# Performance work log

Measured on AMD Instinct MI355X. Metric: run time of the kernel, lower is better.

Reference implementation:

```python
import jax, jax.numpy as jnp
import numpy as np

GRID = 300  # NaiveFourierKANLayer default gridsize
EPS = 1e-5


def layer_norm(x, w, b):
    mu = jnp.mean(x, axis=-1, keepdims=True)
    var = jnp.var(x, axis=-1, keepdims=True)
    return (x - mu) * jax.lax.rsqrt(var + EPS) * w + b


def fourier_kan(x, coeffs, bias):
    # x: [..., I], coeffs: [2, O, I, G], bias: [1, O]
    shp = x.shape
    I = shp[-1]
    xf = x.reshape(-1, I)
    k = jnp.arange(1, GRID + 1, dtype=x.dtype)           # [G]
    arg = xf[:, :, None] * k                             # [B, I, G]
    y = jnp.einsum('big,oig->bo', jnp.cos(arg), coeffs[0])
    y = y + jnp.einsum('big,oig->bo', jnp.sin(arg), coeffs[1])
    y = y + bias                                         # bias broadcasts [1, O]
    return y.reshape(shp[:-1] + (coeffs.shape[1],))


def setup_inputs() -> dict:
    key = jax.random.key(0)
    ks = jax.random.split(key, 4)
    B, N, D = 8, 196, 128          # batch, in_channels, in_dim
    O1 = 2 * D                     # amplifier out_dim
    x = jax.random.normal(ks[0], (B, N, D), dtype=jnp.float32)
    fc1_coeffs = jax.random.normal(ks[1], (2, O1, D, GRID), dtype=jnp.float32) / np.sqrt(D * GRID)
    fc2_coeffs = jax.random.normal(ks[2], (2, N, N, GRID), dtype=jnp.float32) / np.sqrt(N * GRID)
    return {
        'x': x,
        'ln1_w': jnp.ones((D,), jnp.float32),
        'ln1_b': jnp.zeros((D,), jnp.float32),
        'fc1_coeffs': fc1_coeffs,
        'fc1_bias': jnp.zeros((1, O1), jnp.float32),
        'ln2_w': jnp.ones((O1,), jnp.float32),
        'ln2_b': jnp.zeros((O1,), jnp.float32),
        'fc2_coeffs': fc2_coeffs,
        'fc2_bias': jnp.zeros((1, N), jnp.float32),
    }


def reference(x, ln1_w, ln1_b, fc1_coeffs, fc1_bias, ln2_w, ln2_b, fc2_coeffs, fc2_bias):
    B, N, D = x.shape
    # amplifier: LN over in_dim, FourierKAN in_dim -> 2*in_dim
    h = fourier_kan(layer_norm(x, ln1_w, ln1_b), fc1_coeffs, fc1_bias)   # [B, N, 2D]
    # channel_mix: LN over 2*in_dim, transpose, FourierKAN over channels, transpose back
    h = layer_norm(h, ln2_w, ln2_b)
    h = jnp.transpose(h, (0, 2, 1))                                      # [B, 2D, N]
    h = fourier_kan(h, fc2_coeffs, fc2_bias)                             # [B, 2D, N]
    h = jnp.transpose(h, (0, 2, 1))                                      # [B, N, 2D]
    return h.reshape(-1, 2 * N, D)                                       # [B, 2N, D]
```

## Files before the change

### kernel.cpp

```cpp
#include <hip/hip_runtime.h>
#include <math.h>

typedef short short8 __attribute__((ext_vector_type(8)));
typedef float f32x4 __attribute__((ext_vector_type(4)));

#define EPSF 1e-5f

union FragU { uint4 q; unsigned u[4]; short8 v; };

__device__ __forceinline__ unsigned pack_trunc2(float lo_val, float hi_val) {
    return __builtin_amdgcn_perm(__float_as_uint(hi_val), __float_as_uint(lo_val), 0x07060302u);
}
__device__ __forceinline__ float trunc_bf(float x) {
    return __uint_as_float(__float_as_uint(x) & 0xFFFF0000u);
}

__device__ __forceinline__ void gload16_lds(const void* g, void* l) {
    __builtin_amdgcn_global_load_lds(
        (const __attribute__((address_space(1))) void*)g,
        (__attribute__((address_space(3))) void*)l, 16, 0, 0);
}

#define PHASE_BAR() do { \
    asm volatile("s_waitcnt vmcnt(0)" ::: "memory"); \
    __builtin_amdgcn_s_barrier(); \
    __builtin_amdgcn_sched_barrier(0); \
    asm volatile("" ::: "memory"); \
} while (0)

__global__ void ln1_kernel(const float* __restrict__ x, const float* __restrict__ w,
                           const float* __restrict__ b, float* __restrict__ xnT) {
    int r = blockIdx.x;
    int t = threadIdx.x;
    const float* row = x + (size_t)r * 128;
    float v0 = row[t], v1 = row[t + 64];
    float s = v0 + v1, q = v0 * v0 + v1 * v1;
    #pragma unroll
    for (int off = 32; off > 0; off >>= 1) {
        s += __shfl_down(s, off);
        q += __shfl_down(q, off);
    }
    s = __shfl(s, 0); q = __shfl(q, 0);
    float mu = s * (1.f / 128.f);
    float var = q * (1.f / 128.f) - mu * mu;
    float rs = rsqrtf(var + EPSF);
    xnT[(size_t)t * 1792 + r]        = (v0 - mu) * rs * w[t]      + b[t];
    xnT[(size_t)(t + 64) * 1792 + r] = (v1 - mu) * rs * w[t + 64] + b[t + 64];
}

__launch_bounds__(256)
__global__ void fc1_kernel(const float* __restrict__ xnT, const float* __restrict__ coeffs,
                           float* __restrict__ h1, int KS) {
    const int nt = blockIdx.x;
    const int mt = blockIdx.y;
    const int ks = blockIdx.z;
    const int i0 = (ks * 128) / KS, i1 = ((ks + 1) * 128) / KS;
    const int t = threadIdx.x;
    const int wv = t >> 6, ln = t & 63;
    const int q = ln >> 4, col = ln & 15;
    const int mwrow = mt * 256 + wv * 64;

    __shared__ unsigned bhi[128 * 36];
    __shared__ unsigned blo[128 * 36];

    const float* c0 = coeffs;
    const float* c1 = coeffs + (size_t)256 * 128 * 300;

    f32x4 acc[4][8] = {};

    const int srow = t >> 1;
    const int j0 = (t & 1) * 16;
    const int og = nt * 128 + srow;
    const size_t prow = (size_t)og * 128;

    for (int i = i0; i < i1; ++i) {
        float zu[4];
        #pragma unroll
        for (int mf = 0; mf < 4; ++mf) {
            int m = mwrow + mf * 16 + col;
            zu[mf] = (m < 1568) ? xnT[(size_t)i * 1792 + m] : 0.f;
        }
        const float* p0 = c0 + (prow + i) * 300;
        const float* p1 = c1 + (prow + i) * 300;

        for (int c = 0; c < 10; ++c) {
            __syncthreads();
            {
                unsigned hw[16], lw[16];
                #pragma unroll
                for (int k4 = 0; k4 < 4; ++k4) {
                    int g = c * 32 + j0 + k4 * 4;
                    float w0[4], w1[4];
                    if (g + 4 <= 300) {
                        float4 a = *(const float4*)(p0 + g);
                        float4 bb = *(const float4*)(p1 + g);
                        w0[0]=a.x; w0[1]=a.y; w0[2]=a.z; w0[3]=a.w;
                        w1[0]=bb.x; w1[1]=bb.y; w1[2]=bb.z; w1[3]=bb.w;
                    } else {
                        #pragma unroll
                        for (int e = 0; e < 4; ++e) {
                            int gg = g + e; bool ok = gg < 300;
                            w0[e] = ok ? p0[gg] : 0.f;
                            w1[e] = ok ? p1[gg] : 0.f;
                        }
                    }
                    #pragma unroll
                    for (int e = 0; e < 4; ++e) {
                        hw[k4*4+e] = pack_trunc2(w0[e], w1[e]);
                        lw[k4*4+e] = pack_trunc2(w0[e]-trunc_bf(w0[e]), w1[e]-trunc_bf(w1[e]));
                    }
                }
                int base = srow * 36 + j0;
                *(uint4*)&bhi[base]      = make_uint4(hw[0], hw[1], hw[2], hw[3]);
                *(uint4*)&bhi[base + 4]  = make_uint4(hw[4], hw[5], hw[6], hw[7]);
                *(uint4*)&bhi[base + 8]  = make_uint4(hw[8], hw[9], hw[10], hw[11]);
                *(uint4*)&bhi[base + 12] = make_uint4(hw[12], hw[13], hw[14], hw[15]);
                *(uint4*)&blo[base]      = make_uint4(lw[0], lw[1], lw[2], lw[3]);
                *(uint4*)&blo[base + 4]  = make_uint4(lw[4], lw[5], lw[6], lw[7]);
                *(uint4*)&blo[base + 8]  = make_uint4(lw[8], lw[9], lw[10], lw[11]);
                *(uint4*)&blo[base + 12] = make_uint4(lw[12], lw[13], lw[14], lw[15]);
            }
            __syncthreads();
            #pragma unroll
            for (int h = 0; h < 2; ++h) {
                FragU ah[4], al[4];
                #pragma unroll
                for (int mf = 0; mf < 4; ++mf) {
                    #pragma unroll
                    for (int d = 0; d < 4; ++d) {
                        float kf = (float)(c * 32 + h * 16 + q * 4 + d + 1);
                        float a = zu[mf] * kf;
                        float cv = __cosf(a), sv = __sinf(a);
                        ah[mf].u[d] = pack_trunc2(cv, sv);
                        al[mf].u[d] = pack_trunc2(cv - trunc_bf(cv), sv - trunc_bf(sv));
                    }
                }
                #pragma unroll
                for (int nf = 0; nf < 8; ++nf) {
                    int addr = (nf * 16 + col) * 36 + h * 16 + q * 4;
                    FragU bh, bl;
                    bh.q = *(const uint4*)&bhi[addr];
                    bl.q = *(const uint4*)&blo[addr];
                    #pragma unroll
                    for (int mf = 0; mf < 4; ++mf) {
                        acc[mf][nf] = __builtin_amdgcn_mfma_f32_16x16x32_bf16(ah[mf].v, bh.v, acc[mf][nf], 0, 0, 0);
                        acc[mf][nf] = __builtin_amdgcn_mfma_f32_16x16x32_bf16(ah[mf].v, bl.v, acc[mf][nf], 0, 0, 0);
                        acc[mf][nf] = __builtin_amdgcn_mfma_f32_16x16x32_bf16(al[mf].v, bh.v, acc[mf][nf], 0, 0, 0);
                    }
                }
            }
        }
    }
    #pragma unroll
    for (int mf = 0; mf < 4; ++mf) {
        if (mwrow + mf * 16 >= 1568) continue;
        int mbase = mwrow + mf * 16 + q * 4;
        #pragma unroll
        for (int nf = 0; nf < 8; ++nf) {
            int o = nt * 128 + nf * 16 + col;
            #pragma unroll
            for (int r = 0; r < 4; ++r)
                atomicAdd(&h1[(size_t)(mbase + r) * 256 + o], acc[mf][nf][r]);
        }
    }
}

__global__ void ln2_kernel(const float* __restrict__ h1, const float* __restrict__ bias,
                           const float* __restrict__ w, const float* __restrict__ b,
                           float* __restrict__ h1n) {
    int r = blockIdx.x;
    int t = threadIdx.x;
    float v = h1[(size_t)r * 256 + t] + bias[t];
    float s = v, q = v * v;
    #pragma unroll
    for (int off = 32; off > 0; off >>= 1) {
        s += __shfl_down(s, off);
        q += __shfl_down(q, off);
    }
    __shared__ float ss[4], qq[4];
    int wid = t >> 6;
    if ((t & 63) == 0) { ss[wid] = s; qq[wid] = q; }
    __syncthreads();
    float S = ss[0] + ss[1] + ss[2] + ss[3];
    float Q = qq[0] + qq[1] + qq[2] + qq[3];
    float mu = S * (1.f / 256.f);
    float var = Q * (1.f / 256.f) - mu * mu;
    float rs = rsqrtf(var + EPSF);
    h1n[(size_t)r * 256 + t] = (v - mu) * rs * w[t] + b[t];
}

__device__ __forceinline__ void cmul(float& xr, float& xi, float br, float bi) {
    float nr = xr * br - xi * bi;
    float ni = xr * bi + xi * br;
    xr = nr; xi = ni;
}

__launch_bounds__(256, 2)
__global__ void fc2_kernel(const float* __restrict__ h1n, const float* __restrict__ coeffs,
                           float* __restrict__ out, int KS) {
    const int nt = blockIdx.x;
    const int b  = blockIdx.y;
    const int ks = blockIdx.z;
    const int i0 = (ks * 196) / KS, i1 = ((ks + 1) * 196) / KS;
    const int t = threadIdx.x;
    const int wv = t >> 6, ln = t & 63;
    const int q = ln >> 4, col = ln & 15;
    const int cwb = wv * 64;

    __shared__ float ldsf[2 * 2 * 4096];
    char* lds_raw = (char*)&ldsf[0];

    const float* d0 = coeffs;
    const float* d1 = coeffs + (size_t)196 * 196 * 300;

    f32x4 acc[4][8] = {};

    const int rb8  = ln >> 3;
    const int gsub = ((ln & 7) ^ rb8) * 4;
    const unsigned km = (q == 3) ? 0u : 0xFFFFFFFFu;

    auto STAGE = [&](int i, int c, int buf) {
        const int g = c * 32 + gsub;
        const size_t gw = (g + 4 <= 300) ? (size_t)g : 0;
        #pragma unroll
        for (int j = 0; j < 4; ++j) {
            int row = wv * 32 + j * 8 + rb8;
            int og = nt * 128 + row;
            if (og > 195) og = 195;
            size_t go = ((size_t)og * 196 + i) * 300 + gw;
            unsigned lo = (unsigned)buf * 32768u + (unsigned)wv * 4096u + (unsigned)j * 1024u;
            gload16_lds(d0 + go, lds_raw + lo);
            gload16_lds(d1 + go, lds_raw + lo + 16384);
        }
    };

    int cur = 0;
    STAGE(i0, 0, 0);
    for (int i = i0; i < i1; ++i) {
        float Rc[4], Rs[4], E1c[4], E1s[4], E13c[4], E13s[4];
        #pragma unroll
        for (int mf = 0; mf < 4; ++mf) {
            float x = h1n[((size_t)b * 196 + i) * 256 + cwb + mf * 16 + col];
            float c1_ = __cosf(x), s1_ = __sinf(x);
            float c2 = c1_*c1_ - s1_*s1_, s2 = 2.f*c1_*s1_;
            float c4 = c2*c2 - s2*s2,    s4 = 2.f*c2*s2;
            float c8 = c4*c4 - s4*s4,    s8 = 2.f*c4*s4;
            float c12 = c8*c4 - s8*s4,   s12 = c8*s4 + s8*c4;
            float c13 = c12*c1_ - s12*s1_, s13 = c12*s1_ + s12*c1_;
            float rc = c1_, rs = s1_;
            float m4c = (q & 1) ? c4 : 1.f, m4s = (q & 1) ? s4 : 0.f;
            cmul(rc, rs, m4c, m4s);
            float m8c = (q & 2) ? c8 : 1.f, m8s = (q & 2) ? s8 : 0.f;
            cmul(rc, rs, m8c, m8s);
            Rc[mf] = rc; Rs[mf] = rs;
            E1c[mf] = c1_; E1s[mf] = s1_;
            E13c[mf] = c13; E13s[mf] = s13;
        }
        for (int c = 0; c < 10; ++c) {
            PHASE_BAR();
            int ni = i, nc = c + 1;
            if (nc == 10) { nc = 0; ni = i + 1; }
            if (ni < i1) STAGE(ni, nc, cur ^ 1);
            __builtin_amdgcn_sched_barrier(0);
            __builtin_amdgcn_s_setprio(1);
            #pragma unroll
            for (int h = 0; h < 2; ++h) {
                if (h == 1 && c == 9) continue;
                FragU af[4];
                #pragma unroll
                for (int mf = 0; mf < 4; ++mf) {
                    #pragma unroll
                    for (int d = 0; d < 4; ++d) {
                        af[mf].u[d] = pack_trunc2(Rc[mf], Rs[mf]);
                        if (d < 3) cmul(Rc[mf], Rs[mf], E1c[mf], E1s[mf]);
                        else       cmul(Rc[mf], Rs[mf], E13c[mf], E13s[mf]);
                    }
                }
                #pragma unroll
                for (int nf = 0; nf < 8; ++nf) {
                    int row = nf * 16 + col;
                    int pb = cur * 32768 + row * 128 + (((h << 6) | (q << 4)) ^ ((col & 7) << 4));
                    float4 f0 = *(const float4*)(lds_raw + pb);
                    float4 f1 = *(const float4*)(lds_raw + pb + 16384);
                    FragU bf;
                    bf.u[0] = pack_trunc2(f0.x, f1.x);
                    bf.u[1] = pack_trunc2(f0.y, f1.y);
                    bf.u[2] = pack_trunc2(f0.z, f1.z);
                    bf.u[3] = pack_trunc2(f0.w, f1.w);
                    if (c == 9) {
                        bf.u[0] &= km; bf.u[1] &= km; bf.u[2] &= km; bf.u[3] &= km;
                    }
                    #pragma unroll
                    for (int mf = 0; mf < 4; ++mf)
                        acc[mf][nf] = __builtin_amdgcn_mfma_f32_16x16x32_bf16(af[mf].v, bf.v, acc[mf][nf], 0, 0, 0);
                }
            }
            __builtin_amdgcn_s_setprio(0);
            cur ^= 1;
        }
    }
    #pragma unroll
    for (int mf = 0; mf < 4; ++mf) {
        int cbase = cwb + mf * 16 + q * 4;
        #pragma unroll
        for (int nf = 0; nf < 8; ++nf) {
            int o = nt * 128 + nf * 16 + col;
            if (o < 196) {
                #pragma unroll
                for (int r = 0; r < 4; ++r)
                    atomicAdd(&out[((size_t)b * 196 + o) * 256 + cbase + r], acc[mf][nf][r]);
            }
        }
    }
}

__global__ void bias2_kernel(float* __restrict__ out, const float* __restrict__ bias) {
    int idx = blockIdx.x * 256 + threadIdx.x;
    int o = (idx >> 8) % 196;
    out[idx] += bias[o];
}

extern "C" void kernel_launch(void* const* d_in, const int* in_sizes, int n_in,
                              void* d_out, int out_size, void* d_ws, size_t ws_size,
                              hipStream_t stream) {
    const float* x       = (const float*)d_in[0];
    const float* ln1w    = (const float*)d_in[1];
    const float* ln1b    = (const float*)d_in[2];
    const float* fc1c    = (const float*)d_in[3];
    const float* fc1bias = (const float*)d_in[4];
    const float* ln2w    = (const float*)d_in[5];
    const float* ln2b    = (const float*)d_in[6];
    const float* fc2c    = (const float*)d_in[7];
    const float* fc2bias = (const float*)d_in[8];
    float* out = (float*)d_out;

    float* xnT = (float*)d_ws;
    float* h1  = xnT + 229376;
    float* h1n = h1 + 401408;

    hipMemsetAsync(h1, 0, (size_t)401408 * 4, stream);
    hipMemsetAsync(d_out, 0, (size_t)401408 * 4, stream);

    const int ks1 = 36, ks2 = 32;
    ln1_kernel<<<1568, 64, 0, stream>>>(x, ln1w, ln1b, xnT);
    fc1_kernel<<<dim3(2, 7, ks1), 256, 0, stream>>>(xnT, fc1c, h1, ks1);
    ln2_kernel<<<1568, 256, 0, stream>>>(h1, fc1bias, ln2w, ln2b, h1n);
    fc2_kernel<<<dim3(2, 8, ks2), 256, 0, stream>>>(h1n, fc2c, out, ks2);
    bias2_kernel<<<1568, 256, 0, stream>>>(out, fc2bias);
}
```

Measured before the change: 689.3 us.

## Double-buffer fc1 coefficient tiles via async global-to-LDS loads

Replaces the register-staged load, bf16-split and LDS store of the fc1 coefficients with direct global_load_lds transfers into a double-buffered, XOR-swizzled fp32 LDS tile. The next chunk is prefetched while MFMAs run on the current one, and the bf16 hi/lo split moves to the consumer side after the LDS read. The final partial chunk's second half is skipped and the q==3 lanes are masked. The changes aim to hide global-load latency and cut barriers. The cost is more LDS (64KB, which limits occupancy) and redundant split arithmetic done per consumer wave.

```diff
diff --git a/kernel.cpp b/kernel.cpp
--- a/kernel.cpp
+++ b/kernel.cpp
@@ -48,7 +48,7 @@
     xnT[(size_t)(t + 64) * 1792 + r] = (v1 - mu) * rs * w[t + 64] + b[t + 64];
 }
 
-__launch_bounds__(256)
+__launch_bounds__(256, 2)
 __global__ void fc1_kernel(const float* __restrict__ xnT, const float* __restrict__ coeffs,
                            float* __restrict__ h1, int KS) {
     const int nt = blockIdx.x;
@@ -60,19 +60,34 @@
     const int q = ln >> 4, col = ln & 15;
     const int mwrow = mt * 256 + wv * 64;
 
-    __shared__ unsigned bhi[128 * 36];
-    __shared__ unsigned blo[128 * 36];
+    __shared__ float ldsf[2 * 2 * 4096];
+    char* lds_raw = (char*)&ldsf[0];
 
     const float* c0 = coeffs;
     const float* c1 = coeffs + (size_t)256 * 128 * 300;
 
     f32x4 acc[4][8] = {};
 
-    const int srow = t >> 1;
-    const int j0 = (t & 1) * 16;
-    const int og = nt * 128 + srow;
-    const size_t prow = (size_t)og * 128;
-
+    const int rb8  = ln >> 3;
+    const int gsub = ((ln & 7) ^ rb8) * 4;
+    const unsigned km = (q == 3) ? 0u : 0xFFFFFFFFu;
+
+    auto STAGE = [&](int i, int c, int buf) {
+        const int g = c * 32 + gsub;
+        const size_t gw = (g + 4 <= 300) ? (size_t)g : 0;
+        #pragma unroll
+        for (int j = 0; j < 4; ++j) {
+            int row = wv * 32 + j * 8 + rb8;
+            int og = nt * 128 + row;
+            size_t go = ((size_t)og * 128 + i) * 300 + gw;
+            unsigned lo = (unsigned)buf * 32768u + (unsigned)wv * 4096u + (unsigned)j * 1024u;
+            gload16_lds(c0 + go, lds_raw + lo);
+            gload16_lds(c1 + go, lds_raw + lo + 16384);
+        }
+    };
+
+    int cur = 0;
+    STAGE(i0, 0, 0);
     for (int i = i0; i < i1; ++i) {
         float zu[4];
         #pragma unroll
@@ -80,49 +95,16 @@
             int m = mwrow + mf * 16 + col;
             zu[mf] = (m < 1568) ? xnT[(size_t)i * 1792 + m] : 0.f;
         }
-        const float* p0 = c0 + (prow + i) * 300;
-        const float* p1 = c1 + (prow + i) * 300;
-
         for (int c = 0; c < 10; ++c) {
-            __syncthreads();
-            {
-                unsigned hw[16], lw[16];
-                #pragma unroll
-                for (int k4 = 0; k4 < 4; ++k4) {
-                    int g = c * 32 + j0 + k4 * 4;
-                    float w0[4], w1[4];
-                    if (g + 4 <= 300) {
-                        float4 a = *(const float4*)(p0 + g);
-                        float4 bb = *(const float4*)(p1 + g);
-                        w0[0]=a.x; w0[1]=a.y; w0[2]=a.z; w0[3]=a.w;
-                        w1[0]=bb.x; w1[1]=bb.y; w1[2]=bb.z; w1[3]=bb.w;
-                    } else {
-                        #pragma unroll
-                        for (int e = 0; e < 4; ++e) {
-                            int gg = g + e; bool ok = gg < 300;
-                            w0[e] = ok ? p0[gg] : 0.f;
-                            w1[e] = ok ? p1[gg] : 0.f;
-                        }
-                    }
-                    #pragma unroll
-                    for (int e = 0; e < 4; ++e) {
-                        hw[k4*4+e] = pack_trunc2(w0[e], w1[e]);
-                        lw[k4*4+e] = pack_trunc2(w0[e]-trunc_bf(w0[e]), w1[e]-trunc_bf(w1[e]));
-                    }
-                }
-                int base = srow * 36 + j0;
-                *(uint4*)&bhi[base]      = make_uint4(hw[0], hw[1], hw[2], hw[3]);
-                *(uint4*)&bhi[base + 4]  = make_uint4(hw[4], hw[5], hw[6], hw[7]);
-                *(uint4*)&bhi[base + 8]  = make_uint4(hw[8], hw[9], hw[10], hw[11]);
-                *(uint4*)&bhi[base + 12] = make_uint4(hw[12], hw[13], hw[14], hw[15]);
-                *(uint4*)&blo[base]      = make_uint4(lw[0], lw[1], lw[2], lw[3]);
-                *(uint4*)&blo[base + 4]  = make_uint4(lw[4], lw[5], lw[6], lw[7]);
-                *(uint4*)&blo[base + 8]  = make_uint4(lw[8], lw[9], lw[10], lw[11]);
-                *(uint4*)&blo[base + 12] = make_uint4(lw[12], lw[13], lw[14], lw[15]);
-            }
-            __syncthreads();
+            PHASE_BAR();
+            int ni = i, nc = c + 1;
+            if (nc == 10) { nc = 0; ni = i + 1; }
+            if (ni < i1) STAGE(ni, nc, cur ^ 1);
+            __builtin_amdgcn_sched_barrier(0);
+            __builtin_amdgcn_s_setprio(1);
             #pragma unroll
             for (int h = 0; h < 2; ++h) {
+                if (h == 1 && c == 9) continue;
                 FragU ah[4], al[4];
                 #pragma unroll
                 for (int mf = 0; mf < 4; ++mf) {
@@ -137,10 +119,23 @@
                 }
                 #pragma unroll
                 for (int nf = 0; nf < 8; ++nf) {
-                    int addr = (nf * 16 + col) * 36 + h * 16 + q * 4;
+                    int row = nf * 16 + col;
+                    int pb = cur * 32768 + row * 128 + (((h << 6) | (q << 4)) ^ ((col & 7) << 4));
+                    float4 f0 = *(const float4*)(lds_raw + pb);
+                    float4 f1 = *(const float4*)(lds_raw + pb + 16384);
                     FragU bh, bl;
-                    bh.q = *(const uint4*)&bhi[addr];
-                    bl.q = *(const uint4*)&blo[addr];
+                    bh.u[0] = pack_trunc2(f0.x, f1.x);
+                    bh.u[1] = pack_trunc2(f0.y, f1.y);
+                    bh.u[2] = pack_trunc2(f0.z, f1.z);
+                    bh.u[3] = pack_trunc2(f0.w, f1.w);
+                    bl.u[0] = pack_trunc2(f0.x - trunc_bf(f0.x), f1.x - trunc_bf(f1.x));
+                    bl.u[1] = pack_trunc2(f0.y - trunc_bf(f0.y), f1.y - trunc_bf(f1.y));
+                    bl.u[2] = pack_trunc2(f0.z - trunc_bf(f0.z), f1.z - trunc_bf(f1.z));
+                    bl.u[3] = pack_trunc2(f0.w - trunc_bf(f0.w), f1.w - trunc_bf(f1.w));
+                    if (c == 9) {
+                        bh.u[0] &= km; bh.u[1] &= km; bh.u[2] &= km; bh.u[3] &= km;
+                        bl.u[0] &= km; bl.u[1] &= km; bl.u[2] &= km; bl.u[3] &= km;
+                    }
                     #pragma unroll
                     for (int mf = 0; mf < 4; ++mf) {
                         acc[mf][nf] = __builtin_amdgcn_mfma_f32_16x16x32_bf16(ah[mf].v, bh.v, acc[mf][nf], 0, 0, 0);
@@ -149,6 +144,8 @@
                     }
                 }
             }
+            __builtin_amdgcn_s_setprio(0);
+            cur ^= 1;
         }
     }
     #pragma unroll
```

After: 700.6 us. Within noise of the previous version (+1.6%).
